# Optimization experiments

Measured on AMD Instinct MI355X. Metric: run time of the kernel, lower is better.

Reference implementation:

```python
import jax, jax.numpy as jnp
import numpy as np

EPS = 1e-5

def _bn(x, gamma, beta):
    # BatchNorm1d training-mode math: batch mean / biased variance over edge dim
    mean = jnp.mean(x, axis=0)
    var = jnp.mean(jnp.square(x - mean), axis=0)
    return (x - mean) * (gamma / jnp.sqrt(var + EPS)) + beta


def setup_inputs() -> dict:
    key = jax.random.key(0)
    ks = jax.random.split(key, 12)
    n, d, s, h, e = 50000, 256, 32, 128, 500000
    feat = 3 * d + s + 1  # 801
    sc = lambda fan_in: 1.0 / np.sqrt(fan_in)
    return {
        "node_embeddings": jax.random.normal(ks[0], (n, d), jnp.float32),
        "gradient_scores": jax.random.normal(ks[1], (e,), jnp.float32),
        "step_embedding": jax.random.normal(ks[2], (s,), jnp.float32),
        "W1": jax.random.normal(ks[3], (feat, h), jnp.float32) * sc(feat),
        "b1": jnp.zeros((h,), jnp.float32),
        "g1": jnp.ones((h,), jnp.float32),
        "be1": jnp.zeros((h,), jnp.float32),
        "W2": jax.random.normal(ks[4], (h, h // 2), jnp.float32) * sc(h),
        "b2": jnp.zeros((h // 2,), jnp.float32),
        "g2": jnp.ones((h // 2,), jnp.float32),
        "be2": jnp.zeros((h // 2,), jnp.float32),
        "W3": jax.random.normal(ks[5], (h // 2, 1), jnp.float32) * sc(h // 2),
        "b3": jnp.zeros((1,), jnp.float32),
        "edge_index": jax.random.randint(ks[6], (2, e), 0, n, jnp.int64),
    }


def reference(node_embeddings, gradient_scores, step_embedding,
              W1, b1, g1, be1, W2, b2, g2, be2, W3, b3, edge_index):
    src, dst = edge_index[0], edge_index[1]
    h_u = node_embeddings[src]              # [E, d]
    h_v = node_embeddings[dst]              # [E, d]
    edge_diff = jnp.abs(h_u - h_v)          # [E, d]
    E = edge_index.shape[1]
    step = jnp.broadcast_to(step_embedding[None, :], (E, step_embedding.shape[0]))
    feats = jnp.concatenate([h_u, h_v, edge_diff, step, gradient_scores[:, None]], axis=1)
    x = jnp.maximum(feats @ W1 + b1, 0.0)
    x = _bn(x, g1, be1)                     # dropout is identity in eval
    x = jnp.maximum(x @ W2 + b2, 0.0)
    x = _bn(x, g2, be2)
    out = jnp.tanh(x @ W3 + b3)[:, 0]       # [E]
    return out
```

## Files before the change

kernel.cpp:

```cpp
#include <hip/hip_runtime.h>

#define NE 500000
#define DIMK 256
#define H1 128
#define H2 64
#define EPSBN 1e-5f
#define GRID1 512
#define NT1 1954
#define GRID2 512
#define NJOBS2 NT1

typedef _Float16 half8 __attribute__((ext_vector_type(8)));
typedef float f32x4 __attribute__((ext_vector_type(4)));
typedef unsigned short ushort8 __attribute__((ext_vector_type(8)));

typedef const __attribute__((address_space(1))) void* gas1_t;
typedef __attribute__((address_space(3))) void* las3_t;

static __device__ __forceinline__ half8 habs8(half8 x) {
  ushort8 u = __builtin_bit_cast(ushort8, x);
  u &= (unsigned short)0x7FFF;
  return __builtin_bit_cast(half8, u);
}
static __device__ __forceinline__ float h2f(unsigned int u) {
  return (float)__builtin_bit_cast(_Float16, (unsigned short)(u & 0xffff));
}
static __device__ __forceinline__ void gload_lds16(const _Float16* src, _Float16* dst) {
  __builtin_amdgcn_global_load_lds((gas1_t)src, (las3_t)dst, 16, 0, 0);
}

__global__ void k_prep(const float* __restrict__ W1, const float* __restrict__ b1,
                       const float* __restrict__ step, float* __restrict__ c0) {
  const int j = threadIdx.x;
  if (j < H1) {
    float a = b1[j];
#pragma unroll
    for (int tt = 0; tt < 32; ++tt) a += step[tt] * W1[(768 + tt) * H1 + j];
    c0[j] = a;
  }
}

__global__ void k_prep16(const float* __restrict__ emb, _Float16* __restrict__ embh) {
  const int i = (blockIdx.x * 256 + threadIdx.x) * 8;
  const float4 a = *(const float4*)(emb + i);
  const float4 b = *(const float4*)(emb + i + 4);
  half8 h;
  h[0] = (_Float16)a.x; h[1] = (_Float16)a.y; h[2] = (_Float16)a.z; h[3] = (_Float16)a.w;
  h[4] = (_Float16)b.x; h[5] = (_Float16)b.y; h[6] = (_Float16)b.z; h[7] = (_Float16)b.w;
  *(half8*)(embh + i) = h;
}

__global__ void k_prepB(const float* __restrict__ W1, _Float16* __restrict__ bfrag) {
  const int g = blockIdx.x * 256 + threadIdx.x;
  const int lane = g & 63, f = g >> 6;
  const int c = f & 7, kc = (f >> 3) & 7, s = f >> 6;
  const int row0 = s * 256 + kc * 32 + (lane >> 4) * 8;
  const int col = c * 16 + (lane & 15);
  half8 h;
#pragma unroll
  for (int j = 0; j < 8; ++j) h[j] = (_Float16)W1[(row0 + j) * H1 + col];
  *(half8*)(bfrag + (size_t)g * 8) = h;
}

#define STAGE1(q, kcv) do {                                                   \
    _Pragma("unroll")                                                         \
    for (int jj = 0; jj < 6; ++jj) {                                          \
      const int sc = jj * 4 + w;                                              \
      const int ff = (sc >> 3) * 64 + (kcv) * 8 + (sc & 7);                   \
      gload_lds16(bfrag + ((size_t)ff * 64 + lane) * 8,                       \
                  s_B + (size_t)(q) * 12288 + sc * 512);                      \
    }                                                                         \
  } while (0)

__global__ __launch_bounds__(256, 2)
void k_layer1(const _Float16* __restrict__ embh, const void* __restrict__ eidx_raw,
              const float* __restrict__ grad, const float* __restrict__ W1,
              const float* __restrict__ c0, const _Float16* __restrict__ bfrag,
              _Float16* __restrict__ x1, float* __restrict__ p1) {
  __shared__ int s_src[256], s_dst[256];
  __shared__ float s_g[256];
  __shared__ float s_wg[128], s_c0[128], s_sum[128], s_sq[128];
  __shared__ __align__(16) _Float16 s_B[2 * 12288];

  const int t = threadIdx.x, bid = blockIdx.x;
  const int w = t >> 6, lane = t & 63, quad = lane >> 4, m15 = lane & 15;

  if (t < 128) {
    s_wg[t] = W1[800 * H1 + t];
    s_c0[t] = c0[t];
    s_sum[t] = 0.f; s_sq[t] = 0.f;
  }

  const unsigned* ew = (const unsigned*)eidx_raw;
  const bool is64 = ((ew[1] | ew[3] | ew[5] | ew[7]) == 0u);
  const int* e32 = (const int*)eidx_raw;
  const long long* e64 = (const long long*)eidx_raw;

  float st_s[8] = {0, 0, 0, 0, 0, 0, 0, 0}, st_q[8] = {0, 0, 0, 0, 0, 0, 0, 0};

  for (int tile = bid; tile < NT1; tile += GRID1) {
    const int base = tile * 256;
    __syncthreads();
    {
      int e = base + t; if (e >= NE) e = NE - 1;
      if (is64) { s_src[t] = (int)e64[e]; s_dst[t] = (int)e64[NE + e]; }
      else      { s_src[t] = e32[e];      s_dst[t] = e32[NE + e]; }
      s_g[t] = grad[e];
    }
    STAGE1(0, 0);
    __syncthreads();

    const int r0 = w * 64 + m15;
    const _Float16* pu[4];
    const _Float16* pv[4];
#pragma unroll
    for (int r = 0; r < 4; ++r) {
      pu[r] = embh + (size_t)s_src[r0 + r * 16] * DIMK + quad * 8;
      pv[r] = embh + (size_t)s_dst[r0 + r * 16] * DIMK + quad * 8;
    }
    f32x4 acc[4][8];
#pragma unroll
    for (int r = 0; r < 4; ++r)
#pragma unroll
      for (int c = 0; c < 8; ++c) acc[r][c] = (f32x4)0.f;

#pragma unroll 1
    for (int kc = 0; kc < 8; ++kc) {
      if (kc < 7) {
        STAGE1((kc + 1) & 1, kc + 1);
        asm volatile("s_waitcnt vmcnt(6)" ::: "memory");
      } else {
        asm volatile("s_waitcnt vmcnt(0)" ::: "memory");
      }
      __builtin_amdgcn_s_barrier();
      __builtin_amdgcn_sched_barrier(0);

      half8 u[4], v[4], d[4];
#pragma unroll
      for (int r = 0; r < 4; ++r) {
        u[r] = *(const half8*)(pu[r] + kc * 32);
        v[r] = *(const half8*)(pv[r] + kc * 32);
      }
#pragma unroll
      for (int r = 0; r < 4; ++r) d[r] = habs8(u[r] - v[r]);

      const half8* bq = (const half8*)s_B + (size_t)(kc & 1) * 1536 + lane;
#pragma unroll
      for (int c = 0; c < 8; ++c) {
        const half8 bu = bq[c * 64];
        const half8 bv = bq[512 + c * 64];
        const half8 bd = bq[1024 + c * 64];
#pragma unroll
        for (int r = 0; r < 4; ++r)
          acc[r][c] = __builtin_amdgcn_mfma_f32_16x16x32_f16(u[r], bu, acc[r][c], 0, 0, 0);
#pragma unroll
        for (int r = 0; r < 4; ++r)
          acc[r][c] = __builtin_amdgcn_mfma_f32_16x16x32_f16(v[r], bv, acc[r][c], 0, 0, 0);
#pragma unroll
        for (int r = 0; r < 4; ++r)
          acc[r][c] = __builtin_amdgcn_mfma_f32_16x16x32_f16(d[r], bd, acc[r][c], 0, 0, 0);
      }
      __builtin_amdgcn_sched_barrier(0);
      __builtin_amdgcn_s_barrier();
    }
#pragma unroll
    for (int r = 0; r < 4; ++r) {
      const int erow = w * 64 + r * 16 + quad * 4;
#pragma unroll
      for (int c = 0; c < 8; ++c) {
        const int colL = c * 16 + m15;
        const float wgv = s_wg[colL], c0v = s_c0[colL];
#pragma unroll
        for (int reg = 0; reg < 4; ++reg) {
          const int e = base + erow + reg;
          float x = acc[r][c][reg] + s_g[erow + reg] * wgv + c0v;
          x = fmaxf(x, 0.f);
          if (e >= NE) x = 0.f;
          st_s[c] += x; st_q[c] += x * x;
          if (e < NE)
            __builtin_nontemporal_store((_Float16)x, &x1[(size_t)e * H1 + colL]);
        }
      }
    }
  }
  __syncthreads();
#pragma unroll
  for (int c = 0; c < 8; ++c) {
    float a = st_s[c]; a += __shfl_xor(a, 16); a += __shfl_xor(a, 32);
    float b = st_q[c]; b += __shfl_xor(b, 16); b += __shfl_xor(b, 32);
    if (lane < 16) { atomicAdd(&s_sum[c * 16 + m15], a); atomicAdd(&s_sq[c * 16 + m15], b); }
  }
  __syncthreads();
  if (t < 128) {
    p1[t * GRID1 + bid] = s_sum[t];
    p1[128 * GRID1 + t * GRID1 + bid] = s_sq[t];
  }
}

__global__ void k_fin1(const float* __restrict__ p1, const float* __restrict__ g1,
                       const float* __restrict__ be1, const float* __restrict__ W2,
                       const float* __restrict__ b2, float* __restrict__ w2f,
                       float* __restrict__ b2f) {
  __shared__ float s1[128], t1[128];
  const int t = threadIdx.x;
  if (t < 128) {
    float s = 0.f, q = 0.f;
    const float4* rs = (const float4*)(p1 + t * GRID1);
    const float4* rq = (const float4*)(p1 + 128 * GRID1 + t * GRID1);
#pragma unroll 4
    for (int i = 0; i < GRID1 / 4; ++i) {
      float4 a = rs[i]; s += a.x + a.y + a.z + a.w;
      float4 b = rq[i]; q += b.x + b.y + b.z + b.w;
    }
    const float inv = 1.0f / (float)NE;
    float mean = s * inv;
    float var = q * inv - mean * mean;
    float sc = g1[t] * rsqrtf(var + EPSBN);
    s1[t] = sc; t1[t] = be1[t] - mean * sc;
  }
  __syncthreads();
  for (int i = t; i < H1 * H2; i += 256) w2f[i] = s1[i >> 6] * W2[i];
  if (t < 64) {
    float b = b2[t];
    for (int j = 0; j < 128; ++j) b += t1[j] * W2[j * 64 + t];
    b2f[t] = b;
  }
}

__global__ __launch_bounds__(256, 2)
void k_layer2(const _Float16* __restrict__ x1, const float* __restrict__ w2f,
              const float* __restrict__ b2f, _Float16* __restrict__ x2,
              float* __restrict__ p2) {
  __shared__ __align__(16) _Float16 b_lds[8192];
  __shared__ float s_b[64], s_sum[64], s_sq[64];
  const int t = threadIdx.x, bid = blockIdx.x;
  const int w = t >> 6, lane = t & 63, quad = lane >> 4, m15 = lane & 15;

  for (int i = t; i < 8192; i += 256) {
    const int j = i & 7, li = (i >> 3) & 63, f = i >> 9;
    const int c = f & 3, kk = f >> 2;
    const int row = kk * 32 + (li >> 4) * 8 + j;
    const int col = c * 16 + (li & 15);
    b_lds[i] = (_Float16)w2f[row * H2 + col];
  }
  if (t < 64) { s_b[t] = b2f[t]; s_sum[t] = 0.f; s_sq[t] = 0.f; }
  __syncthreads();

  float st_s[4] = {0, 0, 0, 0}, st_q[4] = {0, 0, 0, 0};
  const half8* bp = (const half8*)b_lds;

  for (int job = bid; job < NJOBS2; job += GRID2) {
    const int base = job * 256;
    const _Float16* pa[4];
#pragma unroll
    for (int r = 0; r < 4; ++r) {
      int e = base + w * 64 + r * 16 + m15; if (e >= NE) e = NE - 1;
      pa[r] = x1 + (size_t)e * H1 + quad * 8;
    }
    f32x4 acc[4][4];
#pragma unroll
    for (int r = 0; r < 4; ++r)
#pragma unroll
      for (int c = 0; c < 4; ++c) acc[r][c] = (f32x4)0.f;

#pragma unroll
    for (int kk = 0; kk < 4; ++kk) {
      half8 a[4];
#pragma unroll
      for (int r = 0; r < 4; ++r) a[r] = *(const half8*)(pa[r] + kk * 32);
#pragma unroll
      for (int c = 0; c < 4; ++c) {
        const half8 bf = bp[(kk * 4 + c) * 64 + lane];
#pragma unroll
        for (int r = 0; r < 4; ++r)
          acc[r][c] = __builtin_amdgcn_mfma_f32_16x16x32_f16(a[r], bf, acc[r][c], 0, 0, 0);
      }
    }
#pragma unroll
    for (int r = 0; r < 4; ++r) {
      const int erow = w * 64 + r * 16 + quad * 4;
#pragma unroll
      for (int c = 0; c < 4; ++c) {
        const int colL = c * 16 + m15;
        const float bv = s_b[colL];
#pragma unroll
        for (int reg = 0; reg < 4; ++reg) {
          const int e = base + erow + reg;
          float x = acc[r][c][reg] + bv;
          x = fmaxf(x, 0.f);
          if (e >= NE) x = 0.f;
          st_s[c] += x; st_q[c] += x * x;
          if (e < NE) x2[(size_t)e * H2 + colL] = (_Float16)x;
        }
      }
    }
  }
  __syncthreads();
#pragma unroll
  for (int c = 0; c < 4; ++c) {
    float a = st_s[c]; a += __shfl_xor(a, 16); a += __shfl_xor(a, 32);
    float b = st_q[c]; b += __shfl_xor(b, 16); b += __shfl_xor(b, 32);
    if (lane < 16) { atomicAdd(&s_sum[c * 16 + m15], a); atomicAdd(&s_sq[c * 16 + m15], b); }
  }
  __syncthreads();
  if (t < 64) {
    p2[t * 512 + bid] = s_sum[t];
    p2[64 * 512 + t * 512 + bid] = s_sq[t];
  }
}

__global__ void k_fin2(const float* __restrict__ p2, const float* __restrict__ g2,
                       const float* __restrict__ be2, const float* __restrict__ W3,
                       const float* __restrict__ b3, float* __restrict__ w3f,
                       float* __restrict__ b3f) {
  __shared__ float tp[64];
  const int t = threadIdx.x;
  if (t < 64) {
    float s = 0.f, q = 0.f;
    const float4* rs = (const float4*)(p2 + t * 512);
    const float4* rq = (const float4*)(p2 + 64 * 512 + t * 512);
#pragma unroll 4
    for (int i = 0; i < 128; ++i) {
      float4 a = rs[i]; s += a.x + a.y + a.z + a.w;
      float4 b = rq[i]; q += b.x + b.y + b.z + b.w;
    }
    const float inv = 1.0f / (float)NE;
    float mean = s * inv;
    float var = q * inv - mean * mean;
    float sc = g2[t] * rsqrtf(var + EPSBN);
    float tt = be2[t] - mean * sc;
    w3f[t] = sc * W3[t];
    tp[t] = tt * W3[t];
  }
  __syncthreads();
  if (t == 0) {
    float b = b3[0];
    for (int j = 0; j < 64; ++j) b += tp[j];
    b3f[0] = b;
  }
}

__global__ __launch_bounds__(256)
void k_out(const unsigned short* __restrict__ x2, const float* __restrict__ w3f,
           const float* __restrict__ b3f, float* __restrict__ out) {
  __shared__ float s_w[64];
  __shared__ float s_b;
  const int t = threadIdx.x;
  if (t < 64) s_w[t] = w3f[t];
  if (t == 0) s_b = b3f[0];
  __syncthreads();
  const int gid = blockIdx.x * 256 + t;
  const int e = gid >> 2, p = gid & 3;
  if (e < NE) {
    const uint4* r = (const uint4*)(x2 + (size_t)e * H2 + p * 16);
    float s = 0.f;
#pragma unroll
    for (int i = 0; i < 2; ++i) {
      const uint4 u = r[i];
      const int jb = p * 16 + i * 8;
      s += h2f(u.x) * s_w[jb + 0] + h2f(u.x >> 16) * s_w[jb + 1];
      s += h2f(u.y) * s_w[jb + 2] + h2f(u.y >> 16) * s_w[jb + 3];
      s += h2f(u.z) * s_w[jb + 4] + h2f(u.z >> 16) * s_w[jb + 5];
      s += h2f(u.w) * s_w[jb + 6] + h2f(u.w >> 16) * s_w[jb + 7];
    }
    s += __shfl_xor(s, 1);
    s += __shfl_xor(s, 2);
    if (p == 0) out[e] = tanhf(s + s_b);
  }
}

extern "C" void kernel_launch(void* const* d_in, const int* in_sizes, int n_in,
                              void* d_out, int out_size, void* d_ws, size_t ws_size,
                              hipStream_t stream) {
  const float* emb  = (const float*)d_in[0];
  const float* grad = (const float*)d_in[1];
  const float* step = (const float*)d_in[2];
  const float* W1   = (const float*)d_in[3];
  const float* b1   = (const float*)d_in[4];
  const float* g1   = (const float*)d_in[5];
  const float* be1  = (const float*)d_in[6];
  const float* W2   = (const float*)d_in[7];
  const float* b2   = (const float*)d_in[8];
  const float* g2   = (const float*)d_in[9];
  const float* be2  = (const float*)d_in[10];
  const float* W3   = (const float*)d_in[11];
  const float* b3   = (const float*)d_in[12];
  const void*  eidx = (const void*)d_in[13];
  float* out = (float*)d_out;

  char* ws = (char*)d_ws;
  _Float16* embh  = (_Float16*)(ws + 0);
  _Float16* x2    = (_Float16*)(ws + 0);
  _Float16* bfrag = (_Float16*)(ws + 25600000LL);
  float*    c0    = (float*)(ws + 25796608LL);
  float*    p1    = (float*)(ws + 26000000LL);
  _Float16* x1    = (_Float16*)(ws + 64000000LL);
  float* p2  = (float*)(ws + 192000000LL);
  float* w2f = (float*)(ws + 192524288LL);
  float* b2f = (float*)(ws + 192557056LL);
  float* w3f = (float*)(ws + 192557312LL);
  float* b3f = (float*)(ws + 192557568LL);

  k_prep  <<<1,    256, 0, stream>>>(W1, b1, step, c0);
  k_prep16<<<6250, 256, 0, stream>>>(emb, embh);
  k_prepB <<<48,   256, 0, stream>>>(W1, bfrag);
  k_layer1<<<GRID1,256, 0, stream>>>(embh, eidx, grad, W1, c0, bfrag, x1, p1);
  k_fin1  <<<1,    256, 0, stream>>>(p1, g1, be1, W2, b2, w2f, b2f);
  k_layer2<<<GRID2,256, 0, stream>>>(x1, w2f, b2f, x2, p2);
  k_fin2  <<<1,    128, 0, stream>>>(p2, g2, be2, W3, b3, w3f, b3f);
  k_out   <<<7813, 256, 0, stream>>>((const unsigned short*)x2, w3f, b3f, out);
}
```

Before: 381.8 us.

## Prefetch gathered rows, pack x1 stores, raise layer2 grid and occupancy

Measured after the change: 452.2 us. 18.4% more time.

```diff
diff --git a/kernel.cpp b/kernel.cpp
--- a/kernel.cpp
+++ b/kernel.cpp
@@ -7,7 +7,7 @@
 #define EPSBN 1e-5f
 #define GRID1 512
 #define NT1 1954
-#define GRID2 512
+#define GRID2 768
 #define NJOBS2 NT1
 
 typedef _Float16 half8 __attribute__((ext_vector_type(8)));
@@ -25,9 +25,16 @@
 static __device__ __forceinline__ float h2f(unsigned int u) {
   return (float)__builtin_bit_cast(_Float16, (unsigned short)(u & 0xffff));
 }
+static __device__ __forceinline__ unsigned packf16(float a, float b) {
+  unsigned lo = (unsigned)__builtin_bit_cast(unsigned short, (_Float16)a);
+  unsigned hi = (unsigned)__builtin_bit_cast(unsigned short, (_Float16)b);
+  return lo | (hi << 16);
+}
 static __device__ __forceinline__ void gload_lds16(const _Float16* src, _Float16* dst) {
   __builtin_amdgcn_global_load_lds((gas1_t)src, (las3_t)dst, 16, 0, 0);
 }
+
+#define SB0 __builtin_amdgcn_sched_barrier(0)
 
 __global__ void k_prep(const float* __restrict__ W1, const float* __restrict__ b1,
                        const float* __restrict__ step, float* __restrict__ c0) {
@@ -118,6 +125,12 @@
       pu[r] = embh + (size_t)s_src[r0 + r * 16] * DIMK + quad * 8;
       pv[r] = embh + (size_t)s_dst[r0 + r * 16] * DIMK + quad * 8;
     }
+    half8 u[4], v[4];
+#pragma unroll
+    for (int r = 0; r < 4; ++r) {
+      u[r] = *(const half8*)pu[r];
+      v[r] = *(const half8*)pv[r];
+    }
     f32x4 acc[4][8];
 #pragma unroll
     for (int r = 0; r < 4; ++r)
@@ -128,19 +141,14 @@
     for (int kc = 0; kc < 8; ++kc) {
       if (kc < 7) {
         STAGE1((kc + 1) & 1, kc + 1);
-        asm volatile("s_waitcnt vmcnt(6)" ::: "memory");
+        asm volatile("s_waitcnt vmcnt(14)" ::: "memory");
       } else {
-        asm volatile("s_waitcnt vmcnt(0)" ::: "memory");
+        asm volatile("s_waitcnt vmcnt(8)" ::: "memory");
       }
       __builtin_amdgcn_s_barrier();
-      __builtin_amdgcn_sched_barrier(0);
-
-      half8 u[4], v[4], d[4];
-#pragma unroll
-      for (int r = 0; r < 4; ++r) {
-        u[r] = *(const half8*)(pu[r] + kc * 32);
-        v[r] = *(const half8*)(pv[r] + kc * 32);
-      }
+      SB0;
+
+      half8 d[4];
 #pragma unroll
       for (int r = 0; r < 4; ++r) d[r] = habs8(u[r] - v[r]);
 
@@ -160,25 +168,45 @@
         for (int r = 0; r < 4; ++r)
           acc[r][c] = __builtin_amdgcn_mfma_f32_16x16x32_f16(d[r], bd, acc[r][c], 0, 0, 0);
       }
-      __builtin_amdgcn_sched_barrier(0);
+      SB0;
+      if (kc < 7) {
+#pragma unroll
+        for (int r = 0; r < 4; ++r) {
+          u[r] = *(const half8*)(pu[r] + (kc + 1) * 32);
+          v[r] = *(const half8*)(pv[r] + (kc + 1) * 32);
+        }
+      }
+      SB0;
       __builtin_amdgcn_s_barrier();
     }
 #pragma unroll
     for (int r = 0; r < 4; ++r) {
       const int erow = w * 64 + r * 16 + quad * 4;
+      const int e0 = base + erow;
 #pragma unroll
       for (int c = 0; c < 8; ++c) {
         const int colL = c * 16 + m15;
         const float wgv = s_wg[colL], c0v = s_c0[colL];
+        float xv[4];
 #pragma unroll
         for (int reg = 0; reg < 4; ++reg) {
-          const int e = base + erow + reg;
           float x = acc[r][c][reg] + s_g[erow + reg] * wgv + c0v;
           x = fmaxf(x, 0.f);
-          if (e >= NE) x = 0.f;
+          if (e0 + reg >= NE) x = 0.f;
+          xv[reg] = x;
           st_s[c] += x; st_q[c] += x * x;
-          if (e < NE)
-            __builtin_nontemporal_store((_Float16)x, &x1[(size_t)e * H1 + colL]);
+        }
+        unsigned b01 = packf16(xv[0], xv[1]);
+        unsigned b23 = packf16(xv[2], xv[3]);
+        unsigned q01 = (unsigned)__shfl_xor((int)b01, 1);
+        unsigned q23 = (unsigned)__shfl_xor((int)b23, 1);
+        const int ce = colL & ~1;
+        if (!(m15 & 1)) {
+          if (e0 < NE)     *(unsigned*)(x1 + (size_t)e0 * H1 + ce)       = (b01 & 0xffffu) | (q01 << 16);
+          if (e0 + 1 < NE) *(unsigned*)(x1 + (size_t)(e0 + 1) * H1 + ce) = (b01 >> 16) | (q01 & 0xffff0000u);
+        } else {
+          if (e0 + 2 < NE) *(unsigned*)(x1 + (size_t)(e0 + 2) * H1 + ce) = (q23 & 0xffffu) | (b23 << 16);
+          if (e0 + 3 < NE) *(unsigned*)(x1 + (size_t)(e0 + 3) * H1 + ce) = (q23 >> 16) | (b23 & 0xffff0000u);
         }
       }
     }
@@ -227,7 +255,7 @@
   }
 }
 
-__global__ __launch_bounds__(256, 2)
+__global__ __launch_bounds__(256, 3)
 void k_layer2(const _Float16* __restrict__ x1, const float* __restrict__ w2f,
               const float* __restrict__ b2f, _Float16* __restrict__ x2,
               float* __restrict__ p2) {
@@ -304,8 +332,8 @@
   }
   __syncthreads();
   if (t < 64) {
-    p2[t * 512 + bid] = s_sum[t];
-    p2[64 * 512 + t * 512 + bid] = s_sq[t];
+    p2[t * GRID2 + bid] = s_sum[t];
+    p2[64 * GRID2 + t * GRID2 + bid] = s_sq[t];
   }
 }
 
@@ -317,10 +345,10 @@
   const int t = threadIdx.x;
   if (t < 64) {
     float s = 0.f, q = 0.f;
-    const float4* rs = (const float4*)(p2 + t * 512);
-    const float4* rq = (const float4*)(p2 + 64 * 512 + t * 512);
+    const float4* rs = (const float4*)(p2 + t * GRID2);
+    const float4* rq = (const float4*)(p2 + 64 * GRID2 + t * GRID2);
 #pragma unroll 4
-    for (int i = 0; i < 128; ++i) {
+    for (int i = 0; i < GRID2 / 4; ++i) {
       float4 a = rs[i]; s += a.x + a.y + a.z + a.w;
       float4 b = rq[i]; q += b.x + b.y + b.z + b.w;
     }
```
